# Kernel tuning notes

Hardware: AMD Instinct MI355X
Metric: run time of the kernel (lower is better)

The kernel has to match this reference:

```python
import jax, jax.numpy as jnp
import numpy as np

B, S, D = 1, 4096, 2048
H, KVH, HD = 16, 4, 128  # heads, kv heads, head_dim
ROPE_BASE = 10000.0


def _rope_cos_sin(position_ids):
    # inv_freq: [HD/2]
    inv_freq = 1.0 / (ROPE_BASE ** (jnp.arange(0, HD, 2, dtype=jnp.float32) / HD))
    # freqs: [B, S, HD/2] -> emb: [B, S, HD] (concat(freqs, freqs))
    freqs = position_ids.astype(jnp.float32)[..., None] * inv_freq
    emb = jnp.concatenate([freqs, freqs], axis=-1)
    # [B, 1, S, HD] to broadcast over heads
    return jnp.cos(emb)[:, None, :, :], jnp.sin(emb)[:, None, :, :]


def _rotate_half(x):
    x1, x2 = x[..., : HD // 2], x[..., HD // 2 :]
    return jnp.concatenate([-x2, x1], axis=-1)


def setup_inputs() -> dict:
    key = jax.random.key(0)
    ks = jax.random.split(key, 5)
    s = 0.02
    return {
        "hidden_states": jax.random.normal(ks[0], (B, S, D), jnp.float32),
        "Wq": jax.random.normal(ks[1], (H * HD, D), jnp.float32) * s,
        "Wk": jax.random.normal(ks[2], (KVH * HD, D), jnp.float32) * s,
        "Wv": jax.random.normal(ks[3], (KVH * HD, D), jnp.float32) * s,
        "Wo": jax.random.normal(ks[4], (D, H * HD), jnp.float32) * s,
        "position_ids": jnp.arange(S, dtype=jnp.int64 if jax.config.jax_enable_x64 else jnp.int32)[None, :].repeat(B, 0),
    }


def reference(hidden_states, Wq, Wk, Wv, Wo, position_ids):
    b, s, _ = hidden_states.shape
    # projections (no bias): [b, s, nheads*hd] -> [b, nh, s, hd]
    q = (hidden_states @ Wq.T).reshape(b, s, H, HD).transpose(0, 2, 1, 3)
    k = (hidden_states @ Wk.T).reshape(b, s, KVH, HD).transpose(0, 2, 1, 3)
    v = (hidden_states @ Wv.T).reshape(b, s, KVH, HD).transpose(0, 2, 1, 3)

    cos, sin = _rope_cos_sin(position_ids)  # [b,1,s,hd]
    q = q * cos + _rotate_half(q) * sin
    k = k * cos + _rotate_half(k) * sin

    # GQA: repeat kv heads (repeat_interleave along head dim)
    n_rep = H // KVH
    k = jnp.repeat(k, n_rep, axis=1)
    v = jnp.repeat(v, n_rep, axis=1)

    # eager quadratic attention with causal mask
    scores = jnp.einsum("bhqd,bhkd->bhqk", q, k) / jnp.sqrt(jnp.float32(HD))
    causal = jnp.tril(jnp.ones((s, s), dtype=bool))
    scores = jnp.where(causal[None, None], scores, jnp.finfo(scores.dtype).min)
    attn = jax.nn.softmax(scores, axis=-1)
    out = jnp.einsum("bhqk,bhkd->bhqd", attn, v)  # [b,h,s,hd]
    out = out.transpose(0, 2, 1, 3).reshape(b, s, H * HD)
    return out @ Wo.T
```

## Files before the change

### kernel.cpp

```cpp
#include <hip/hip_runtime.h>
#include <hip/hip_bf16.h>

constexpr int S   = 4096;
constexpr int D   = 2048;
constexpr int H   = 16;
constexpr int KVH = 4;
constexpr int HD  = 128;

using short8 = __attribute__((ext_vector_type(8))) short;
using f32x4  = __attribute__((ext_vector_type(4))) float;
using f32x16 = __attribute__((ext_vector_type(16))) float;

__device__ inline ushort f2bf(float f) {
  union { float f; unsigned u; } x{f};
  unsigned r = x.u + 0x7FFFu + ((x.u >> 16) & 1u);
  return (ushort)(r >> 16);
}
__device__ inline float bf2f(ushort h) {
  union { unsigned u; float f; } x{(unsigned)h << 16};
  return x.f;
}
__device__ inline unsigned pkbf(float a, float b) {
  union { float f; unsigned u; } xa{a}, xb{b};
  unsigned ra = xa.u + 0x7FFFu + ((xa.u >> 16) & 1u);
  unsigned rb = xb.u + 0x7FFFu + ((xb.u >> 16) & 1u);
#if __has_builtin(__builtin_amdgcn_perm)
  return __builtin_amdgcn_perm(rb, ra, 0x07060302u);
#else
  return (rb & 0xFFFF0000u) | (ra >> 16);
#endif
}
__device__ inline unsigned pkbf_t(float a, float b) {
  union { float f; unsigned u; } xa{a}, xb{b};
#if __has_builtin(__builtin_amdgcn_perm)
  return __builtin_amdgcn_perm(xb.u, xa.u, 0x07060302u);
#else
  return (xb.u & 0xFFFF0000u) | (xa.u >> 16);
#endif
}
__device__ inline float fast_exp2(float x) {
#if __has_builtin(__builtin_amdgcn_exp2f)
  return __builtin_amdgcn_exp2f(x);
#else
  return exp2f(x);
#endif
}

__device__ inline void swap_half(unsigned a, unsigned b, unsigned& x, unsigned& y) {
#if __has_builtin(__builtin_amdgcn_permlane32_swap)
  using uint2v = __attribute__((ext_vector_type(2))) unsigned;
  uint2v r = __builtin_amdgcn_permlane32_swap(a, b, false, false);
  x = r[0]; y = r[1];
#else
  unsigned bx = __shfl_xor(b, 32), ax = __shfl_xor(a, 32);
  int p = (threadIdx.x & 63) >> 5;
  x = p ? bx : a;
  y = p ? b : ax;
#endif
}

__device__ inline void async_copy16(const ushort* g, ushort* l) {
  __builtin_amdgcn_global_load_lds(
      (const __attribute__((address_space(1))) unsigned int*)g,
      (__attribute__((address_space(3))) unsigned int*)l, 16, 0, 0);
}

constexpr size_t N_HID = (size_t)S * D;
constexpr size_t N_WQ  = (size_t)(H * HD) * D;
constexpr size_t N_WKV = (size_t)(KVH * HD) * D;
constexpr size_t C1_ = N_HID;
constexpr size_t C2_ = C1_ + N_WQ;
constexpr size_t C3_ = C2_ + N_WKV;
constexpr size_t C4_ = C3_ + N_WKV;
constexpr size_t C5_ = C4_ + N_WQ;

__global__ void cvt_all_kernel(const float* __restrict__ hid, const float* __restrict__ wq,
                               const float* __restrict__ wk, const float* __restrict__ wv,
                               const float* __restrict__ wo, ushort* __restrict__ dst) {
  size_t i = (size_t)blockIdx.x * blockDim.x + threadIdx.x;
  size_t off = i * 4;
  if (off >= C5_) return;
  const float* src;
  if      (off < C1_) src = hid + off;
  else if (off < C2_) src = wq + (off - C1_);
  else if (off < C3_) src = wk + (off - C2_);
  else if (off < C4_) src = wv + (off - C3_);
  else                src = wo + (off - C4_);
  float4 f = *(const float4*)src;
  ushort4 o;
  o.x = f2bf(f.x); o.y = f2bf(f.y); o.z = f2bf(f.z); o.w = f2bf(f.w);
  *(ushort4*)&dst[off] = o;
}

template <int OUT_MODE>
__device__ __forceinline__ void gemm_tile(const ushort* __restrict__ A,
                                          const ushort* __restrict__ Bt,
                                          void* __restrict__ Cv,
                                          int M, int N, int K, int bxi, int byi,
                                          ushort* As, ushort* Bs) {
  const int bm = byi * 128;
  const int bn = bxi * 128;
  const int tid  = threadIdx.x;
  const int lane = tid & 63;
  const int w    = tid >> 6;
  const int wr = w >> 1, wc = w & 1;
  const int lm = lane & 15, quad = lane >> 4;

  f32x4 acc[4][4];
#pragma unroll
  for (int i = 0; i < 4; ++i)
#pragma unroll
    for (int j = 0; j < 4; ++j) acc[i][j] = (f32x4){0.f, 0.f, 0.f, 0.f};

  for (int k0 = 0; k0 < K; k0 += 32) {
#pragma unroll
    for (int j = 0; j < 2; ++j) {
      int idx = j * 256 + tid;
      int row = idx >> 2;
      int col = (idx & 3) * 8;
      int ubase = (j * 256 + w * 64) * 8;
      async_copy16(A + (size_t)(bm + row) * K + k0 + col, &As[ubase]);
      async_copy16(Bt + (size_t)(bn + row) * K + k0 + col, &Bs[ubase]);
    }
    __syncthreads();
    short8 af[4], bfr[4];
#pragma unroll
    for (int t = 0; t < 4; ++t) {
      af[t]  = *(const short8*)&As[(wr * 64 + t * 16 + lm) * 32 + quad * 8];
      bfr[t] = *(const short8*)&Bs[(wc * 64 + t * 16 + lm) * 32 + quad * 8];
    }
#pragma unroll
    for (int i = 0; i < 4; ++i)
#pragma unroll
      for (int j = 0; j < 4; ++j)
        acc[i][j] = __builtin_amdgcn_mfma_f32_16x16x32_bf16(af[i], bfr[j], acc[i][j], 0, 0, 0);
    __syncthreads();
  }

#pragma unroll
  for (int i = 0; i < 4; ++i)
#pragma unroll
    for (int j = 0; j < 4; ++j) {
      if (OUT_MODE == 2) {
        int col  = bn + wc * 64 + j * 16 + lm;
        int rowb = bm + wr * 64 + i * 16 + quad * 4;
        ushort4 o4;
        o4.x = f2bf(acc[i][j][0]); o4.y = f2bf(acc[i][j][1]);
        o4.z = f2bf(acc[i][j][2]); o4.w = f2bf(acc[i][j][3]);
        *(ushort4*)&((ushort*)Cv)[(size_t)col * M + rowb] = o4;
      } else {
#pragma unroll
        for (int r = 0; r < 4; ++r) {
          size_t row = bm + wr * 64 + i * 16 + quad * 4 + r;
          size_t col = bn + wc * 64 + j * 16 + lm;
          if (OUT_MODE == 1) ((ushort*)Cv)[row * N + col] = f2bf(acc[i][j][r]);
          else               ((float*)Cv)[row * N + col]  = acc[i][j][r];
        }
      }
    }
}

__global__ __launch_bounds__(256) void gemm_qkv_kernel(const ushort* __restrict__ hb,
                                                       const ushort* __restrict__ wq,
                                                       const ushort* __restrict__ wk,
                                                       const ushort* __restrict__ wv,
                                                       ushort* __restrict__ qb,
                                                       ushort* __restrict__ kb,
                                                       ushort* __restrict__ vtb) {
  __shared__ __align__(16) ushort As[128 * 32];
  __shared__ __align__(16) ushort Bs[128 * 32];
  int bid = blockIdx.x;
  if (bid < 512) {
    gemm_tile<1>(hb, wq, qb, S, H * HD, D, bid & 15, bid >> 4, As, Bs);
  } else if (bid < 640) {
    int b = bid - 512;
    gemm_tile<1>(hb, wk, kb, S, KVH * HD, D, b & 3, b >> 2, As, Bs);
  } else {
    int b = bid - 640;
    gemm_tile<2>(hb, wv, vtb, S, KVH * HD, D, b & 3, b >> 2, As, Bs);
  }
}

template <int OUT_MODE>
__global__ __launch_bounds__(256) void gemm_bt_kernel(const ushort* __restrict__ A,
                                                      const ushort* __restrict__ Bt,
                                                      void* __restrict__ Cv,
                                                      int M, int N, int K) {
  __shared__ __align__(16) ushort As[128 * 32];
  __shared__ __align__(16) ushort Bs[128 * 32];
  gemm_tile<OUT_MODE>(A, Bt, Cv, M, N, K, blockIdx.x, blockIdx.y, As, Bs);
}

__global__ void rope_bf16_kernel(ushort* __restrict__ qb, ushort* __restrict__ kb,
                                 const int* __restrict__ pos_ids) {
  int idx = blockIdx.x * blockDim.x + threadIdx.x;
  const int total = S * (H + KVH) * (HD / 2);
  if (idx >= total) return;
  int j = idx & 63;
  int t = idx >> 6;
  int head = t % (H + KVH);
  int s = t / (H + KVH);
  float p = (float)pos_ids[s];
  float inv_freq = exp2f(-(float)j * (13.287712379549449f / 64.0f));
  float ang = p * inv_freq;
  float c = cosf(ang), sn = sinf(ang);
  ushort* base = (head < H) ? (qb + (size_t)s * (H * HD) + head * HD)
                            : (kb + (size_t)s * (KVH * HD) + (head - H) * HD);
  float x1 = bf2f(base[j]), x2 = bf2f(base[j + 64]);
  base[j]      = f2bf(x1 * c - x2 * sn);
  base[j + 64] = f2bf(x2 * c + x1 * sn);
}

__global__ __launch_bounds__(512) void attn_mfma_kernel(const ushort* __restrict__ q,
                                                        const ushort* __restrict__ k,
                                                        const ushort* __restrict__ Vt,
                                                        ushort* __restrict__ o) {
  const int bid = blockIdx.x;
  const int h   = 2 * (bid & 7) + ((bid >> 3) & 1);
  const int t   = bid >> 4;
  const int qi  = 31 - t;
  const int q0  = qi * 128;
  const int kvh = h >> 2;
  const int tid  = threadIdx.x;
  const int lane = tid & 63;
  const int w    = tid >> 6;
  const int qw   = w >> 1;
  const int ks   = w & 1;
  const int m32  = lane & 31;
  const int p    = lane >> 5;

  __shared__ __align__(16) ushort LDSu[32768];

  const int q0w = q0 + qw * 32;

  short8 qf[8];
#pragma unroll
  for (int s = 0; s < 8; ++s)
    qf[s] = *(const short8*)&q[(size_t)(q0w + m32) * (H * HD) + h * HD + s * 16 + p * 8];

  f32x16 Oacc[4];
#pragma unroll
  for (int i = 0; i < 4; ++i)
#pragma unroll
    for (int r = 0; r < 16; ++r) Oacc[i][r] = 0.f;
  float ls4[4] = {0.f, 0.f, 0.f, 0.f};

  auto stage = [&](int k0s, int buf) {
#pragma unroll
    for (int i = 0; i < 4; ++i) {
      int c = w * 4 + i;
      if (c < 16) {
        int kh = c >> 3, s = c & 7;
        async_copy16(&k[(size_t)(k0s + kh * 32 + m32) * (KVH * HD) + kvh * HD + s * 16 + p * 8],
                     &LDSu[buf * 8192 + c * 512]);
      } else {
        int cv = c - 16;
        int ht = cv >> 2, t2 = cv & 3;
        async_copy16(&Vt[(size_t)(kvh * HD + ht * 32 + m32) * S + k0s + t2 * 16 + p * 8],
                     &LDSu[16384 + buf * 8192 + cv * 512]);
      }
    }
  };

  stage(0, 0);
  __syncthreads();

  const float C1  = 0.08838834764831845f * 1.4426950408889634f;
  const float F2n = -12.0f * 1.4426950408889634f;
  const int T = 2 * qi + 2;

  for (int tt = 0; tt < T; ++tt) {
    const int k0  = tt * 64;
    const int cur = tt & 1;
    if (tt + 1 < T) stage(k0 + 64, cur ^ 1);
    const ushort* Kb = &LDSu[cur * 8192];
    const ushort* Vb = &LDSu[16384 + cur * 8192];

    const int kbase = k0 + ks * 32;
    if (kbase <= q0w + 31) {
      f32x16 stA, stB;
#pragma unroll
      for (int r = 0; r < 16; ++r) { stA[r] = 0.f; stB[r] = 0.f; }
#pragma unroll
      for (int s = 0; s < 8; s += 2) {
        short8 kf0 = *(const short8*)&Kb[(ks * 8 + s) * 512 + lane * 8];
        short8 kf1 = *(const short8*)&Kb[(ks * 8 + s + 1) * 512 + lane * 8];
        stA = __builtin_amdgcn_mfma_f32_32x32x16_bf16(kf0, qf[s], stA, 0, 0, 0);
        stB = __builtin_amdgcn_mfma_f32_32x32x16_bf16(kf1, qf[s + 1], stB, 0, 0, 0);
      }

      float pv[16];
      if (kbase == q0w) {
#pragma unroll
        for (int r = 0; r < 16; ++r) {
          int kvl = (r & 3) + 8 * (r >> 2) + 4 * p;
          float e = fast_exp2(fmaf(stA[r] + stB[r], C1, F2n));
          e = (kvl > m32) ? 0.f : e;
          pv[r] = e; ls4[r & 3] += e;
        }
      } else {
#pragma unroll
        for (int r = 0; r < 16; ++r) {
          float e = fast_exp2(fmaf(stA[r] + stB[r], C1, F2n));
          pv[r] = e; ls4[r & 3] += e;
        }
      }

      unsigned own2[4][2];
#pragma unroll
      for (int g = 0; g < 4; ++g) {
        own2[g][0] = pkbf_t(pv[4 * g + 0], pv[4 * g + 1]);
        own2[g][1] = pkbf_t(pv[4 * g + 2], pv[4 * g + 3]);
      }
      short8 pf[2];
#pragma unroll
      for (int t2 = 0; t2 < 2; ++t2) {
        unsigned x0, y0, x1, y1;
        swap_half(own2[2 * t2][0], own2[2 * t2 + 1][0], x0, y0);
        swap_half(own2[2 * t2][1], own2[2 * t2 + 1][1], x1, y1);
        union { unsigned u4[4]; short8 s8; } pb;
        pb.u4[0] = x0; pb.u4[1] = x1; pb.u4[2] = y0; pb.u4[3] = y1;
        pf[t2] = pb.s8;
      }

#pragma unroll
      for (int ht = 0; ht < 4; ++ht)
#pragma unroll
        for (int t2l = 0; t2l < 2; ++t2l) {
          int cv = ht * 4 + ks * 2 + t2l;
          short8 vf = *(const short8*)&Vb[cv * 512 + lane * 8];
          Oacc[ht] = __builtin_amdgcn_mfma_f32_32x32x16_bf16(vf, pf[t2l], Oacc[ht], 0, 0, 0);
        }
    }
    __syncthreads();
  }

  float lsum = (ls4[0] + ls4[1]) + (ls4[2] + ls4[3]);
  float* mb = (float*)LDSu;

  if (ks) mb[(qw << 6) | lane] = lsum;
  __syncthreads();
  if (!ks) lsum += mb[(qw << 6) | lane];
  __syncthreads();

  if (ks) {
    float* base = mb + qw * 4096;
#pragma unroll
    for (int ht = 0; ht < 4; ++ht)
#pragma unroll
      for (int r = 0; r < 16; ++r)
        base[ht * 1024 + r * 64 + lane] = Oacc[ht][r];
  }
  __syncthreads();

  if (!ks) {
    const float* base = mb + qw * 4096;
#pragma unroll
    for (int ht = 0; ht < 4; ++ht)
#pragma unroll
      for (int r = 0; r < 16; ++r)
        Oacc[ht][r] += base[ht * 1024 + r * 64 + lane];

    float ltot = lsum + __shfl_xor(lsum, 32);
    float inv = 1.0f / ltot;
#pragma unroll
    for (int ht = 0; ht < 4; ++ht)
#pragma unroll
      for (int rq = 0; rq < 4; ++rq) {
        uint2 dd;
        dd.x = pkbf(Oacc[ht][4 * rq + 0] * inv, Oacc[ht][4 * rq + 1] * inv);
        dd.y = pkbf(Oacc[ht][4 * rq + 2] * inv, Oacc[ht][4 * rq + 3] * inv);
        *(uint2*)&o[(size_t)(q0w + m32) * (H * HD) + h * HD + ht * 32 + 8 * rq + 4 * p] = dd;
      }
  }
}

extern "C" void kernel_launch(void* const* d_in, const int* in_sizes, int n_in,
                              void* d_out, int out_size, void* d_ws, size_t ws_size,
                              hipStream_t stream) {
  const float* hidden = (const float*)d_in[0];
  const float* Wq     = (const float*)d_in[1];
  const float* Wk     = (const float*)d_in[2];
  const float* Wv     = (const float*)d_in[3];
  const float* Wo     = (const float*)d_in[4];
  const int*   pos    = (const int*)d_in[5];
  float* out = (float*)d_out;

  ushort* hb  = (ushort*)d_ws;
  ushort* wqb = hb  + N_HID;
  ushort* wkb = wqb + N_WQ;
  ushort* wvb = wkb + N_WKV;
  ushort* wob = wvb + N_WKV;
  ushort* qb  = wob + N_WQ;
  ushort* kb  = qb  + (size_t)S * (H * HD);
  ushort* vtb = kb  + (size_t)S * (KVH * HD);
  ushort* ob  = vtb + (size_t)(KVH * HD) * S;

  dim3 blk(256);
  size_t n4 = C5_ / 4;
  cvt_all_kernel<<<(int)((n4 + 255) / 256), blk, 0, stream>>>(hidden, Wq, Wk, Wv, Wo, hb);

  gemm_qkv_kernel<<<dim3(768), blk, 0, stream>>>(hb, wqb, wkb, wvb, qb, kb, vtb);

  int rope_total = S * (H + KVH) * (HD / 2);
  rope_bf16_kernel<<<(rope_total + 255) / 256, blk, 0, stream>>>(qb, kb, pos);

  attn_mfma_kernel<<<dim3(512), dim3(512), 0, stream>>>(qb, kb, vtb, ob);

  gemm_bt_kernel<0><<<dim3(D / 128, S / 128), blk, 0, stream>>>(ob, wob, out, S, D, D);
}
```

Before: 343.7 us.

## Fuse Q RoPE into attention loads and precompute cos/sin table

Adds a kernel that precomputes a per-position cos/sin table, and applies RoPE to Q inside the attention kernel right after the Q fragments are loaded, so Q is no longer read and rewritten by a separate pass. A smaller rope kernel now rotates only the K heads using the table. This removes most of the standalone RoPE memory traffic and the repeated transcendental evaluation. In exchange it adds an extra kernel launch and per-thread table reads in the attention prologue.

Result: no change. 345.9 us (+0.6%).

```diff
diff --git a/kernel.cpp b/kernel.cpp
--- a/kernel.cpp
+++ b/kernel.cpp
@@ -90,6 +90,31 @@
   ushort4 o;
   o.x = f2bf(f.x); o.y = f2bf(f.y); o.z = f2bf(f.z); o.w = f2bf(f.w);
   *(ushort4*)&dst[off] = o;
+}
+
+__global__ void trig_table_kernel(const int* __restrict__ pos, float2* __restrict__ tab) {
+  int idx = blockIdx.x * 256 + threadIdx.x;
+  if (idx >= S * 64) return;
+  int s = idx >> 6, j2 = idx & 63;
+  float invf = exp2f(-(float)j2 * (13.287712379549449f / 64.0f));
+  float ang = (float)pos[s] * invf;
+  float2 cs; cs.x = cosf(ang); cs.y = sinf(ang);
+  tab[idx] = cs;
+}
+
+__global__ void rope_k_kernel(ushort* __restrict__ kb, const float2* __restrict__ tab) {
+  int idx = blockIdx.x * 256 + threadIdx.x;
+  const int total = S * KVH * 64;
+  if (idx >= total) return;
+  int j = idx & 63;
+  int t = idx >> 6;
+  int kvh_i = t & 3;
+  int srow  = t >> 2;
+  ushort* base = kb + (size_t)srow * (KVH * HD) + kvh_i * HD;
+  float2 cs = tab[(size_t)srow * 64 + j];
+  float x1 = bf2f(base[j]), x2 = bf2f(base[j + 64]);
+  base[j]      = f2bf(x1 * cs.x - x2 * cs.y);
+  base[j + 64] = f2bf(x2 * cs.x + x1 * cs.y);
 }
 
 template <int OUT_MODE>
@@ -191,30 +216,11 @@
   gemm_tile<OUT_MODE>(A, Bt, Cv, M, N, K, blockIdx.x, blockIdx.y, As, Bs);
 }
 
-__global__ void rope_bf16_kernel(ushort* __restrict__ qb, ushort* __restrict__ kb,
-                                 const int* __restrict__ pos_ids) {
-  int idx = blockIdx.x * blockDim.x + threadIdx.x;
-  const int total = S * (H + KVH) * (HD / 2);
-  if (idx >= total) return;
-  int j = idx & 63;
-  int t = idx >> 6;
-  int head = t % (H + KVH);
-  int s = t / (H + KVH);
-  float p = (float)pos_ids[s];
-  float inv_freq = exp2f(-(float)j * (13.287712379549449f / 64.0f));
-  float ang = p * inv_freq;
-  float c = cosf(ang), sn = sinf(ang);
-  ushort* base = (head < H) ? (qb + (size_t)s * (H * HD) + head * HD)
-                            : (kb + (size_t)s * (KVH * HD) + (head - H) * HD);
-  float x1 = bf2f(base[j]), x2 = bf2f(base[j + 64]);
-  base[j]      = f2bf(x1 * c - x2 * sn);
-  base[j + 64] = f2bf(x2 * c + x1 * sn);
-}
-
 __global__ __launch_bounds__(512) void attn_mfma_kernel(const ushort* __restrict__ q,
                                                         const ushort* __restrict__ k,
                                                         const ushort* __restrict__ Vt,
-                                                        ushort* __restrict__ o) {
+                                                        ushort* __restrict__ o,
+                                                        const float2* __restrict__ tab) {
   const int bid = blockIdx.x;
   const int h   = 2 * (bid & 7) + ((bid >> 3) & 1);
   const int t   = bid >> 4;
@@ -238,6 +244,21 @@
   for (int s = 0; s < 8; ++s)
     qf[s] = *(const short8*)&q[(size_t)(q0w + m32) * (H * HD) + h * HD + s * 16 + p * 8];
 
+  {
+    const float2* trow = tab + (size_t)(q0w + m32) * 64 + p * 8;
+#pragma unroll
+    for (int s = 0; s < 4; ++s) {
+#pragma unroll
+      for (int j = 0; j < 8; ++j) {
+        float2 cs = trow[s * 16 + j];
+        float lo = bf2f((ushort)qf[s][j]);
+        float hi = bf2f((ushort)qf[s + 4][j]);
+        qf[s][j]     = (short)f2bf(lo * cs.x - hi * cs.y);
+        qf[s + 4][j] = (short)f2bf(hi * cs.x + lo * cs.y);
+      }
+    }
+  }
+
   f32x16 Oacc[4];
 #pragma unroll
   for (int i = 0; i < 4; ++i)
@@ -395,17 +416,19 @@
   ushort* kb  = qb  + (size_t)S * (H * HD);
   ushort* vtb = kb  + (size_t)S * (KVH * HD);
   ushort* ob  = vtb + (size_t)(KVH * HD) * S;
+  float2* tab = (float2*)(ob + (size_t)S * (H * HD));
 
   dim3 blk(256);
   size_t n4 = C5_ / 4;
   cvt_all_kernel<<<(int)((n4 + 255) / 256), blk, 0, stream>>>(hidden, Wq, Wk, Wv, Wo, hb);
 
+  trig_table_kernel<<<(S * 64 + 255) / 256, blk, 0, stream>>>(pos, tab);
+
   gemm_qkv_kernel<<<dim3(768), blk, 0, stream>>>(hb, wqb, wkb, wvb, qb, kb, vtb);
 
-  int rope_total = S * (H + KVH) * (HD / 2);
-  rope_bf16_kernel<<<(rope_total + 255) / 256, blk, 0, stream>>>(qb, kb, pos);
-
-  attn_mfma_kernel<<<dim3(512), dim3(512), 0, stream>>>(qb, kb, vtb, ob);
+  rope_k_kernel<<<(S * KVH * 64 + 255) / 256, blk, 0, stream>>>(kb, tab);
+
+  attn_mfma_kernel<<<dim3(512), dim3(512), 0, stream>>>(qb, kb, vtb, ob, tab);
 
   gemm_bt_kernel<0><<<dim3(D / 128, S / 128), blk, 0, stream>>>(ob, wob, out, S, D, D);
 }
```
